# Optimization experiments

Hardware: AMD Instinct MI355X
Metric: run time of the kernel (lower is better)

## Reference

```python
import jax, jax.numpy as jnp
import numpy as np

INPUT_DIM = 128
OUTPUT_DIM = 128
FEATURE_DIM = 2 * OUTPUT_DIM            # 256
EDGE_DIM = 2 * FEATURE_DIM              # 512
H_DIM = INPUT_DIM + FEATURE_DIM + 2 * EDGE_DIM  # input + xp + (mean,max) pooled
N_INTT = 50000
N_MVTX = 50000
N_EDGES = 320000


def _linear_params(key, fan_in, fan_out):
    kw, kb = jax.random.split(key)
    lim = 1.0 / np.sqrt(fan_in)
    W = jax.random.uniform(kw, (fan_in, fan_out), jnp.float32, -lim, lim)
    b = jax.random.uniform(kb, (fan_out,), jnp.float32, -lim, lim)
    return W, b


def setup_inputs() -> dict:
    key = jax.random.key(0)
    ks = jax.random.split(key, 10)
    x_intt = jax.random.normal(ks[0], (N_INTT, INPUT_DIM), jnp.float32)
    x_mvtx = jax.random.normal(ks[1], (N_MVTX, INPUT_DIM), jnp.float32)
    start = jax.random.randint(ks[2], (N_EDGES,), 0, N_INTT)
    end = jax.random.randint(ks[3], (N_EDGES,), 0, N_MVTX)
    edge_index = jnp.stack([start, end], axis=0).astype(jnp.int64) if jax.config.jax_enable_x64 else jnp.stack([start, end], axis=0)
    W_in_intt, b_in_intt = _linear_params(ks[4], INPUT_DIM, FEATURE_DIM)
    W_in_mvtx, b_in_mvtx = _linear_params(ks[5], INPUT_DIM, FEATURE_DIM)
    W_score, b_score = _linear_params(ks[6], EDGE_DIM, 1)
    W_out_intt, b_out_intt = _linear_params(ks[7], H_DIM, OUTPUT_DIM)
    W_out_mvtx, b_out_mvtx = _linear_params(ks[8], H_DIM, OUTPUT_DIM)
    return {
        "x_intt": x_intt, "x_mvtx": x_mvtx, "edge_index": edge_index,
        "W_in_intt": W_in_intt, "b_in_intt": b_in_intt,
        "W_in_mvtx": W_in_mvtx, "b_in_mvtx": b_in_mvtx,
        "W_score": W_score, "b_score": b_score,
        "W_out_intt": W_out_intt, "b_out_intt": b_out_intt,
        "W_out_mvtx": W_out_mvtx, "b_out_mvtx": b_out_mvtx,
    }


def _scatter_mean(edges, idx, n):
    # torch_scatter.scatter_mean with out=zeros: sum / max(count, 1)
    s = jax.ops.segment_sum(edges, idx, num_segments=n)
    cnt = jax.ops.segment_sum(jnp.ones((edges.shape[0], 1), edges.dtype), idx, num_segments=n)
    return s / jnp.maximum(cnt, 1.0)


def _scatter_max(edges, idx, n):
    # torch_scatter.scatter_max with out=zeros: out participates in the max -> clamp at 0
    m = jax.ops.segment_max(edges, idx, num_segments=n)
    return jnp.maximum(m, 0.0)


def reference(x_intt, x_mvtx, edge_index,
              W_in_intt, b_in_intt, W_in_mvtx, b_in_mvtx,
              W_score, b_score, W_out_intt, b_out_intt,
              W_out_mvtx, b_out_mvtx):
    xp_intt = x_intt @ W_in_intt + b_in_intt          # [Ni, F]
    xp_mvtx = x_mvtx @ W_in_mvtx + b_in_mvtx          # [Nm, F]
    start, end = edge_index[0], edge_index[1]
    xp = jnp.concatenate([xp_intt[start], xp_mvtx[end]], axis=-1)  # [E, 2F]
    # aggregator_activation = 'potential': exp(-|x|)
    score = jnp.exp(-jnp.abs(xp @ W_score + b_score))  # [E, 1]
    edges = xp * score                                 # [E, 2F]

    mean_intt = _scatter_mean(edges, start, x_intt.shape[0])
    max_intt = _scatter_max(edges, start, x_intt.shape[0])
    mean_mvtx = _scatter_mean(edges, end, x_mvtx.shape[0])
    max_mvtx = _scatter_max(edges, end, x_mvtx.shape[0])

    H_intt = jnp.concatenate([x_intt, xp_intt, mean_intt, max_intt], axis=-1)
    H_mvtx = jnp.concatenate([x_mvtx, xp_mvtx, mean_mvtx, max_mvtx], axis=-1)
    h_intt = jax.nn.relu(H_intt @ W_out_intt + b_out_intt)
    h_mvtx = jax.nn.relu(H_mvtx @ W_out_mvtx + b_out_mvtx)
    return (h_intt, h_mvtx)
```

## Files before the change

### kernel.cpp

```cpp
#include <hip/hip_runtime.h>


typedef __attribute__((ext_vector_type(8))) short bf16x8;
typedef __attribute__((ext_vector_type(4))) float f32x4;

static __device__ __forceinline__ unsigned short f2bf(float f) {
  unsigned int u = __float_as_uint(f);
  u = (u + 0x7FFFu + ((u >> 16) & 1u)) >> 16;
  return (unsigned short)u;
}
static __device__ __forceinline__ float bf2f(unsigned short s) {
  return __uint_as_float(((unsigned int)s) << 16);
}

#define GLD16(gp, lp)                                                        \
  __builtin_amdgcn_global_load_lds(                                          \
      (const __attribute__((address_space(1))) void*)(gp),                   \
      (__attribute__((address_space(3))) void*)(lp), 16, 0, 0)

__global__ void k_prep_wt(const float* __restrict__ Wo,
                          unsigned short* __restrict__ Wt, int K, int Ncol) {
  int idx = blockIdx.x * blockDim.x + threadIdx.x;
  if (idx >= K * Ncol) return;
  int k = idx / Ncol, c = idx % Ncol;
  Wt[(size_t)c * K + k] = f2bf(Wo[idx]);
}

__global__ __launch_bounds__(256) void k_gemm_in(
    const float* __restrict__ x, const unsigned short* __restrict__ Wint,
    const float* __restrict__ bias, const float* __restrict__ Wsc,
    unsigned short* __restrict__ xp, float* __restrict__ a_out, int N) {
  __shared__ __align__(16) unsigned short Ab[64 * 16 * 8];
  __shared__ __align__(16) unsigned short Bb[256 * 16 * 8];
  const int tid = threadIdx.x;
  const int l = tid & 63;
  const int lr = l & 15, lg = l >> 4;
  const int w = tid >> 6, wr = w >> 1, wc = w & 1;
  const int r0 = blockIdx.x * 64;
  const int wbase = tid & 192;

#pragma unroll
  for (int i = 0; i < 16; ++i) {
    int g = i * 256 + tid;
    int row = g >> 4, c = g & 15;
    int sc = c ^ (row & 7);
    GLD16(Wint + (size_t)row * 128 + sc * 8,
          &Bb[(size_t)(i * 256 + wbase) * 8]);
  }
#pragma unroll
  for (int i = 0; i < 4; ++i) {
    int g = i * 256 + tid;
    int row = g >> 4, c = g & 15;
    int ar = min(r0 + row, N - 1);
    const float* src = x + (size_t)ar * 128 + c * 8;
    float4 u = *(const float4*)src;
    float4 v = *(const float4*)(src + 4);
    bf16x8 h;
    h[0] = (short)f2bf(u.x); h[1] = (short)f2bf(u.y);
    h[2] = (short)f2bf(u.z); h[3] = (short)f2bf(u.w);
    h[4] = (short)f2bf(v.x); h[5] = (short)f2bf(v.y);
    h[6] = (short)f2bf(v.z); h[7] = (short)f2bf(v.w);
    *(bf16x8*)&Ab[(size_t)(row * 16 + (c ^ (row & 7))) * 8] = h;
  }
  __syncthreads();

  f32x4 acc[2][8];
#pragma unroll
  for (int m = 0; m < 2; ++m)
#pragma unroll
    for (int t = 0; t < 8; ++t) {
      f32x4 z = {0.f, 0.f, 0.f, 0.f};
      acc[m][t] = z;
    }
#pragma unroll
  for (int kk = 0; kk < 4; ++kk) {
    int chq = kk * 4 + lg;
    bf16x8 a[2], bt[8];
#pragma unroll
    for (int m = 0; m < 2; ++m) {
      int row = wr * 32 + m * 16 + lr;
      a[m] = *(const bf16x8*)&Ab[(row * 16 + (chq ^ (row & 7))) * 8];
    }
#pragma unroll
    for (int t = 0; t < 8; ++t) {
      int row = wc * 128 + t * 16 + lr;
      bt[t] = *(const bf16x8*)&Bb[(row * 16 + (chq ^ (row & 7))) * 8];
    }
#pragma unroll
    for (int m = 0; m < 2; ++m)
#pragma unroll
      for (int t = 0; t < 8; ++t)
        acc[m][t] = __builtin_amdgcn_mfma_f32_16x16x32_bf16(
            a[m], bt[t], acc[m][t], 0, 0, 0);
  }

  float wscv[8], bb[8];
#pragma unroll
  for (int t = 0; t < 8; ++t) {
    int c = wc * 128 + t * 16 + lr;
    wscv[t] = Wsc[c];
    bb[t] = bias[c];
  }
#pragma unroll
  for (int m = 0; m < 2; ++m) {
    int rb = r0 + wr * 32 + m * 16 + lg * 4;
    float p0 = 0.f, p1 = 0.f, p2 = 0.f, p3 = 0.f;
#pragma unroll
    for (int t = 0; t < 8; ++t) {
      int c = wc * 128 + t * 16 + lr;
      float v0 = acc[m][t][0] + bb[t];
      float v1 = acc[m][t][1] + bb[t];
      float v2 = acc[m][t][2] + bb[t];
      float v3 = acc[m][t][3] + bb[t];
      if (rb + 0 < N) xp[(size_t)(rb + 0) * 256 + c] = f2bf(v0);
      if (rb + 1 < N) xp[(size_t)(rb + 1) * 256 + c] = f2bf(v1);
      if (rb + 2 < N) xp[(size_t)(rb + 2) * 256 + c] = f2bf(v2);
      if (rb + 3 < N) xp[(size_t)(rb + 3) * 256 + c] = f2bf(v3);
      p0 = fmaf(v0, wscv[t], p0); p1 = fmaf(v1, wscv[t], p1);
      p2 = fmaf(v2, wscv[t], p2); p3 = fmaf(v3, wscv[t], p3);
    }
#pragma unroll
    for (int off = 1; off < 16; off <<= 1) {
      p0 += __shfl_xor(p0, off); p1 += __shfl_xor(p1, off);
      p2 += __shfl_xor(p2, off); p3 += __shfl_xor(p3, off);
    }
    if (lr == 0) {
      if (rb + 0 < N) atomicAdd(a_out + rb + 0, p0);
      if (rb + 1 < N) atomicAdd(a_out + rb + 1, p1);
      if (rb + 2 < N) atomicAdd(a_out + rb + 2, p2);
      if (rb + 3 < N) atomicAdd(a_out + rb + 3, p3);
    }
  }
}

__global__ void k_deg(const int* __restrict__ es, const int* __restrict__ ee,
                      int E, int* __restrict__ deg_i, int* __restrict__ deg_m) {
  int e = blockIdx.x * blockDim.x + threadIdx.x;
  if (e >= E) return;
  atomicAdd(deg_i + es[e], 1);
  atomicAdd(deg_m + ee[e], 1);
}

__global__ __launch_bounds__(256) void k_scan_blk(
    const int* __restrict__ deg, int* __restrict__ blksum, int n) {
  __shared__ int sm[256];
  int t = threadIdx.x;
  int i = blockIdx.x * 256 + t;
  sm[t] = (i < n) ? deg[i] : 0;
  __syncthreads();
#pragma unroll
  for (int off = 128; off; off >>= 1) {
    if (t < off) sm[t] += sm[t + off];
    __syncthreads();
  }
  if (t == 0) blksum[blockIdx.x] = sm[0];
}

__global__ __launch_bounds__(1024) void k_scan_top(
    const int* __restrict__ bs_i, int* __restrict__ bb_i, int nbi,
    const int* __restrict__ bs_m, int* __restrict__ bb_m, int nbm) {
  const int* bs = blockIdx.x ? bs_m : bs_i;
  int* bb = blockIdx.x ? bb_m : bb_i;
  int nb = blockIdx.x ? nbm : nbi;
  __shared__ int sm[1024];
  int t = threadIdx.x;
  int d = (t < nb) ? bs[t] : 0;
  sm[t] = d;
  __syncthreads();
  for (int off = 1; off < 1024; off <<= 1) {
    int v = (t >= off) ? sm[t - off] : 0;
    __syncthreads();
    sm[t] += v;
    __syncthreads();
  }
  if (t < nb) bb[t] = sm[t] - d;
}

__global__ __launch_bounds__(256) void k_scan_wr(
    const int* __restrict__ deg, const int* __restrict__ blkbase,
    int* __restrict__ rp, int* __restrict__ cur, int n, int E) {
  __shared__ int sm[256];
  int t = threadIdx.x;
  int i = blockIdx.x * 256 + t;
  int d = (i < n) ? deg[i] : 0;
  sm[t] = d;
  __syncthreads();
  for (int off = 1; off < 256; off <<= 1) {
    int v = (t >= off) ? sm[t - off] : 0;
    __syncthreads();
    sm[t] += v;
    __syncthreads();
  }
  if (i < n) {
    int v = blkbase[blockIdx.x] + sm[t] - d;
    rp[i] = v; cur[i] = v;
  }
  if (i == 0) rp[n] = E;
}

__global__ void k_fill(const int* __restrict__ es, const int* __restrict__ ee,
                       int E, const float* __restrict__ a_i,
                       const float* __restrict__ a_m,
                       const float* __restrict__ bsc,
                       int* __restrict__ cur_i, int* __restrict__ col_i,
                       float* __restrict__ sv_i,
                       int* __restrict__ cur_m, int* __restrict__ col_m,
                       float* __restrict__ sv_m) {
  int e = blockIdx.x * blockDim.x + threadIdx.x;
  if (e >= E) return;
  int s = es[e], m = ee[e];
  float sc = expf(-fabsf(a_i[s] + a_m[m] + bsc[0]));
  int pi = atomicAdd(cur_i + s, 1);
  col_i[pi] = m; sv_i[pi] = sc;
  int pm = atomicAdd(cur_m + m, 1);
  col_m[pm] = s; sv_m[pm] = sc;
}

__global__ __launch_bounds__(256) void k_agg(
    const unsigned short* __restrict__ xp_oth,
    const int* __restrict__ rowptr, const int* __restrict__ col,
    const float* __restrict__ sv, unsigned short* __restrict__ Hg,
    float4* __restrict__ scal, int base, int cnt) {
  int local = blockIdx.x * 4 + (threadIdx.x >> 6);
  if (local >= cnt) return;
  int node = base + local;
  int l = threadIdx.x & 63;

  float sum_s = 0.f, mx_s = -1e30f, mn_s = 1e30f;
  float sv0 = 0.f, sv1 = 0.f, sv2 = 0.f, sv3 = 0.f;
  float mv0 = -1e30f, mv1 = -1e30f, mv2 = -1e30f, mv3 = -1e30f;
  int jb = rowptr[node], je = rowptr[node + 1];
  int dg = je - jb;
  int j = jb;
  for (; j + 3 < je; j += 4) {
    int o0 = col[j], o1 = col[j + 1], o2 = col[j + 2], o3 = col[j + 3];
    float s0 = sv[j], s1 = sv[j + 1], s2 = sv[j + 2], s3 = sv[j + 3];
    ushort4 g0 = *(const ushort4*)(xp_oth + (size_t)o0 * 256 + 4 * l);
    ushort4 g1 = *(const ushort4*)(xp_oth + (size_t)o1 * 256 + 4 * l);
    ushort4 g2 = *(const ushort4*)(xp_oth + (size_t)o2 * 256 + 4 * l);
    ushort4 g3 = *(const ushort4*)(xp_oth + (size_t)o3 * 256 + 4 * l);
    float f0, f1, f2, f3;
    f0 = bf2f(g0.x); f1 = bf2f(g0.y); f2 = bf2f(g0.z); f3 = bf2f(g0.w);
    sv0 = fmaf(s0, f0, sv0); sv1 = fmaf(s0, f1, sv1);
    sv2 = fmaf(s0, f2, sv2); sv3 = fmaf(s0, f3, sv3);
    mv0 = fmaxf(mv0, s0 * f0); mv1 = fmaxf(mv1, s0 * f1);
    mv2 = fmaxf(mv2, s0 * f2); mv3 = fmaxf(mv3, s0 * f3);
    f0 = bf2f(g1.x); f1 = bf2f(g1.y); f2 = bf2f(g1.z); f3 = bf2f(g1.w);
    sv0 = fmaf(s1, f0, sv0); sv1 = fmaf(s1, f1, sv1);
    sv2 = fmaf(s1, f2, sv2); sv3 = fmaf(s1, f3, sv3);
    mv0 = fmaxf(mv0, s1 * f0); mv1 = fmaxf(mv1, s1 * f1);
    mv2 = fmaxf(mv2, s1 * f2); mv3 = fmaxf(mv3, s1 * f3);
    f0 = bf2f(g2.x); f1 = bf2f(g2.y); f2 = bf2f(g2.z); f3 = bf2f(g2.w);
    sv0 = fmaf(s2, f0, sv0); sv1 = fmaf(s2, f1, sv1);
    sv2 = fmaf(s2, f2, sv2); sv3 = fmaf(s2, f3, sv3);
    mv0 = fmaxf(mv0, s2 * f0); mv1 = fmaxf(mv1, s2 * f1);
    mv2 = fmaxf(mv2, s2 * f2); mv3 = fmaxf(mv3, s2 * f3);
    f0 = bf2f(g3.x); f1 = bf2f(g3.y); f2 = bf2f(g3.z); f3 = bf2f(g3.w);
    sv0 = fmaf(s3, f0, sv0); sv1 = fmaf(s3, f1, sv1);
    sv2 = fmaf(s3, f2, sv2); sv3 = fmaf(s3, f3, sv3);
    mv0 = fmaxf(mv0, s3 * f0); mv1 = fmaxf(mv1, s3 * f1);
    mv2 = fmaxf(mv2, s3 * f2); mv3 = fmaxf(mv3, s3 * f3);
    sum_s += (s0 + s1) + (s2 + s3);
    mx_s = fmaxf(mx_s, fmaxf(fmaxf(s0, s1), fmaxf(s2, s3)));
    mn_s = fminf(mn_s, fminf(fminf(s0, s1), fminf(s2, s3)));
  }
  for (; j < je; ++j) {
    int o0 = col[j];
    float s0 = sv[j];
    ushort4 g0 = *(const ushort4*)(xp_oth + (size_t)o0 * 256 + 4 * l);
    float f0 = bf2f(g0.x), f1 = bf2f(g0.y), f2 = bf2f(g0.z), f3 = bf2f(g0.w);
    sv0 = fmaf(s0, f0, sv0); sv1 = fmaf(s0, f1, sv1);
    sv2 = fmaf(s0, f2, sv2); sv3 = fmaf(s0, f3, sv3);
    mv0 = fmaxf(mv0, s0 * f0); mv1 = fmaxf(mv1, s0 * f1);
    mv2 = fmaxf(mv2, s0 * f2); mv3 = fmaxf(mv3, s0 * f3);
    sum_s += s0; mx_s = fmaxf(mx_s, s0); mn_s = fminf(mn_s, s0);
  }
  float inv = 1.f / (float)(dg > 0 ? dg : 1);
  unsigned short* Hr = Hg + (size_t)local * 512;
  *(ushort4*)(Hr + 4 * l) = make_ushort4(
      f2bf(sv0 * inv), f2bf(sv1 * inv), f2bf(sv2 * inv), f2bf(sv3 * inv));
  *(ushort4*)(Hr + 256 + 4 * l) = make_ushort4(
      f2bf(fmaxf(mv0, 0.f)), f2bf(fmaxf(mv1, 0.f)),
      f2bf(fmaxf(mv2, 0.f)), f2bf(fmaxf(mv3, 0.f)));
  if (l == 0)
    scal[local] = make_float4(sum_s * inv, dg > 0 ? mx_s : 0.f,
                              dg > 0 ? mn_s : 0.f, 0.f);
}

__global__ __launch_bounds__(512) void k_gemm_out(
    const float* __restrict__ x, const unsigned short* __restrict__ xp,
    const unsigned short* __restrict__ Hg, const float4* __restrict__ scal,
    const unsigned short* __restrict__ Wt, const float* __restrict__ bias,
    float* __restrict__ out, int Nloc, int own_first) {
  __shared__ unsigned short Ab[2][64 * 64];
  __shared__ unsigned short Bb[2][128 * 64];
  const int tid = threadIdx.x;
  const int l = tid & 63;
  const int lr = l & 15, lg = l >> 4;
  const int w = tid >> 6;
  const int wr = w >> 2, wc = w & 3;
  const int r0 = blockIdx.x * 64;
  const int wbase = tid & 448;

  const int arow = tid >> 3, ac = tid & 7;
  const int ar = min(r0 + arow, Nloc - 1);
  const int asc = ac ^ (arow & 7);
  unsigned short* adst_reg = &Ab[0][(size_t)(arow * 8 + asc) * 8];
  const size_t adst_off = (size_t)(arow * 8 + asc) * 8;
  float4 s4 = scal[ar];
  const float ss = s4.x, mxs = s4.y, mns = s4.z;

  f32x4 acc[2][2];
#pragma unroll
  for (int m = 0; m < 2; ++m)
#pragma unroll
    for (int t = 0; t < 2; ++t) {
      f32x4 z = {0.f, 0.f, 0.f, 0.f};
      acc[m][t] = z;
    }

  auto stage = [&](int b, int t) {
    if (t < 2) {
      const float* src = x + (size_t)ar * 128 + t * 64 + ac * 8;
      float4 u = *(const float4*)src;
      float4 v = *(const float4*)(src + 4);
      bf16x8 h;
      h[0] = (short)f2bf(u.x); h[1] = (short)f2bf(u.y);
      h[2] = (short)f2bf(u.z); h[3] = (short)f2bf(u.w);
      h[4] = (short)f2bf(v.x); h[5] = (short)f2bf(v.y);
      h[6] = (short)f2bf(v.z); h[7] = (short)f2bf(v.w);
      *(bf16x8*)&Ab[b][adst_off] = h;
    } else if (t < 6) {
      GLD16(xp + (size_t)ar * 256 + (t - 2) * 64 + asc * 8,
            &Ab[b][(size_t)wbase * 8]);
    } else {
      int phase = (t - 6) >> 2, sub = (t - 6) & 3;
      int is_own = own_first ? !(phase & 1) : (phase & 1);
      if (is_own) {
        bf16x8 v = *(const bf16x8*)(xp + (size_t)ar * 256 + sub * 64 + ac * 8);
        bf16x8 h;
        if (phase < 2) {
#pragma unroll
          for (int i = 0; i < 8; ++i)
            h[i] = (short)f2bf(bf2f((unsigned short)v[i]) * ss);
        } else {
#pragma unroll
          for (int i = 0; i < 8; ++i) {
            float f = bf2f((unsigned short)v[i]);
            h[i] = (short)f2bf(fmaxf(fmaxf(f * mxs, f * mns), 0.f));
          }
        }
        *(bf16x8*)&Ab[b][adst_off] = h;
      } else {
        int hoff = (phase >= 2 ? 256 : 0) + sub * 64;
        GLD16(Hg + (size_t)ar * 512 + hoff + asc * 8,
              &Ab[b][(size_t)wbase * 8]);
      }
    }
    int kb = t * 64;
#pragma unroll
    for (int i = 0; i < 2; ++i) {
      int g = i * 512 + tid;
      int row = g >> 3, c = g & 7;
      int sc = c ^ (row & 7);
      GLD16(Wt + (size_t)row * 1408 + kb + sc * 8,
            &Bb[b][(size_t)(i * 512 + wbase) * 8]);
    }
  };

  auto compute = [&](int b) {
#pragma unroll
    for (int kk = 0; kk < 2; ++kk) {
      int chq = kk * 4 + lg;
      bf16x8 a[2], bt[2];
#pragma unroll
      for (int m = 0; m < 2; ++m) {
        int row = wr * 32 + m * 16 + lr;
        a[m] = *(const bf16x8*)&Ab[b][(row * 8 + (chq ^ (row & 7))) * 8];
      }
#pragma unroll
      for (int t = 0; t < 2; ++t) {
        int row = wc * 32 + t * 16 + lr;
        bt[t] = *(const bf16x8*)&Bb[b][(row * 8 + (chq ^ (row & 7))) * 8];
      }
#pragma unroll
      for (int m = 0; m < 2; ++m)
#pragma unroll
        for (int t = 0; t < 2; ++t)
          acc[m][t] = __builtin_amdgcn_mfma_f32_16x16x32_bf16(
              a[m], bt[t], acc[m][t], 0, 0, 0);
    }
  };

  stage(0, 0);
  __syncthreads();
  int cur = 0;
  for (int t = 0; t < 22; ++t) {
    if (t < 21) stage(cur ^ 1, t + 1);
    compute(cur);
    __syncthreads();
    cur ^= 1;
  }

#pragma unroll
  for (int m = 0; m < 2; ++m) {
    int rb = r0 + wr * 32 + m * 16 + lg * 4;
#pragma unroll
    for (int t = 0; t < 2; ++t) {
      int c = wc * 32 + t * 16 + lr;
      float bbias = bias[c];
#pragma unroll
      for (int r = 0; r < 4; ++r) {
        int rr = rb + r;
        if (rr < Nloc) out[(size_t)rr * 128 + c] = fmaxf(acc[m][t][r] + bbias, 0.f);
      }
    }
  }
}

extern "C" void kernel_launch(void* const* d_in, const int* in_sizes, int n_in,
                              void* d_out, int out_size, void* d_ws,
                              size_t ws_size, hipStream_t stream) {
  const float* x_i  = (const float*)d_in[0];
  const float* x_m  = (const float*)d_in[1];
  const int*   ei   = (const int*)d_in[2];
  const float* Wi_i = (const float*)d_in[3];
  const float* bi_i = (const float*)d_in[4];
  const float* Wi_m = (const float*)d_in[5];
  const float* bi_m = (const float*)d_in[6];
  const float* Wsc  = (const float*)d_in[7];
  const float* bsc  = (const float*)d_in[8];
  const float* Wo_i = (const float*)d_in[9];
  const float* bo_i = (const float*)d_in[10];
  const float* Wo_m = (const float*)d_in[11];
  const float* bo_m = (const float*)d_in[12];
  float* out = (float*)d_out;

  int Ni = in_sizes[0] / 128, Nm = in_sizes[1] / 128, E = in_sizes[2] / 2;
  const int* es = ei;
  const int* ee = ei + E;
  int nbi = (Ni + 255) / 256, nbm = (Nm + 255) / 256;

  char* p = (char*)d_ws;
  auto alloc = [&](size_t bytes) {
    char* q = p;
    p += (bytes + 255) & ~(size_t)255;
    return q;
  };
  unsigned short* xp_i = (unsigned short*)alloc((size_t)Ni * 256 * 2);
  unsigned short* xp_m = (unsigned short*)alloc((size_t)Nm * 256 * 2);
  float* a_i   = (float*)alloc((size_t)Ni * 4);
  float* a_m   = (float*)alloc((size_t)Nm * 4);
  int* deg_i   = (int*)alloc((size_t)Ni * 4);
  int* deg_m   = (int*)alloc((size_t)Nm * 4);
  int* rp_i    = (int*)alloc((size_t)(Ni + 1) * 4);
  int* rp_m    = (int*)alloc((size_t)(Nm + 1) * 4);
  int* cur_i   = (int*)alloc((size_t)Ni * 4);
  int* cur_m   = (int*)alloc((size_t)Nm * 4);
  int* bs_i    = (int*)alloc((size_t)nbi * 4);
  int* bs_m    = (int*)alloc((size_t)nbm * 4);
  int* bb_i    = (int*)alloc((size_t)nbi * 4);
  int* bb_m    = (int*)alloc((size_t)nbm * 4);
  int* col_i   = (int*)alloc((size_t)E * 4);
  int* col_m   = (int*)alloc((size_t)E * 4);
  float* sv_i  = (float*)alloc((size_t)E * 4);
  float* sv_m  = (float*)alloc((size_t)E * 4);
  unsigned short* Wt_i = (unsigned short*)alloc((size_t)128 * 1408 * 2);
  unsigned short* Wt_m = (unsigned short*)alloc((size_t)128 * 1408 * 2);
  unsigned short* Wint_i = (unsigned short*)alloc((size_t)256 * 128 * 2);
  unsigned short* Wint_m = (unsigned short*)alloc((size_t)256 * 128 * 2);

  size_t used = (size_t)(p - (char*)d_ws);
  if (used + 256 > ws_size) return;
  size_t avail = ws_size - used - 256;
  long long srows_ll = (long long)(avail / 1040);
  int maxN = (Ni > Nm ? Ni : Nm);
  int maxPad = (maxN + 127) & ~127;
  int S = (int)(srows_ll > maxPad ? maxPad : srows_ll);
  S &= ~127;
  if (S < 128) return;
  unsigned short* Hg = (unsigned short*)alloc((size_t)S * 512 * 2);
  float4* scal = (float4*)alloc((size_t)S * 16);

  hipMemsetAsync(deg_i, 0, (size_t)Ni * 4, stream);
  hipMemsetAsync(deg_m, 0, (size_t)Nm * 4, stream);
  hipMemsetAsync(a_i, 0, (size_t)Ni * 4, stream);
  hipMemsetAsync(a_m, 0, (size_t)Nm * 4, stream);

  k_prep_wt<<<(1408 * 128 + 255) / 256, 256, 0, stream>>>(Wo_i, Wt_i, 1408, 128);
  k_prep_wt<<<(1408 * 128 + 255) / 256, 256, 0, stream>>>(Wo_m, Wt_m, 1408, 128);
  k_prep_wt<<<(128 * 256 + 255) / 256, 256, 0, stream>>>(Wi_i, Wint_i, 128, 256);
  k_prep_wt<<<(128 * 256 + 255) / 256, 256, 0, stream>>>(Wi_m, Wint_m, 128, 256);

  k_gemm_in<<<(Ni + 63) / 64, 256, 0, stream>>>(x_i, Wint_i, bi_i, Wsc, xp_i, a_i, Ni);
  k_gemm_in<<<(Nm + 63) / 64, 256, 0, stream>>>(x_m, Wint_m, bi_m, Wsc + 256, xp_m, a_m, Nm);

  k_deg<<<(E + 255) / 256, 256, 0, stream>>>(es, ee, E, deg_i, deg_m);
  k_scan_blk<<<nbi, 256, 0, stream>>>(deg_i, bs_i, Ni);
  k_scan_blk<<<nbm, 256, 0, stream>>>(deg_m, bs_m, Nm);
  k_scan_top<<<2, 1024, 0, stream>>>(bs_i, bb_i, nbi, bs_m, bb_m, nbm);
  k_scan_wr<<<nbi, 256, 0, stream>>>(deg_i, bb_i, rp_i, cur_i, Ni, E);
  k_scan_wr<<<nbm, 256, 0, stream>>>(deg_m, bb_m, rp_m, cur_m, Nm, E);
  k_fill<<<(E + 255) / 256, 256, 0, stream>>>(es, ee, E, a_i, a_m, bsc,
                                              cur_i, col_i, sv_i,
                                              cur_m, col_m, sv_m);

  for (int base = 0; base < Ni; base += S) {
    int cnt = Ni - base; if (cnt > S) cnt = S;
    k_agg<<<(cnt + 3) / 4, 256, 0, stream>>>(xp_m, rp_i, col_i, sv_i,
                                             Hg, scal, base, cnt);
    k_gemm_out<<<(cnt + 63) / 64, 512, 0, stream>>>(
        x_i + (size_t)base * 128, xp_i + (size_t)base * 256, Hg, scal,
        Wt_i, bo_i, out + (size_t)base * 128, cnt, 1);
  }
  float* out_m = out + (size_t)Ni * 128;
  for (int base = 0; base < Nm; base += S) {
    int cnt = Nm - base; if (cnt > S) cnt = S;
    k_agg<<<(cnt + 3) / 4, 256, 0, stream>>>(xp_i, rp_m, col_m, sv_m,
                                             Hg, scal, base, cnt);
    k_gemm_out<<<(cnt + 63) / 64, 512, 0, stream>>>(
        x_m + (size_t)base * 128, xp_m + (size_t)base * 256, Hg, scal,
        Wt_m, bo_m, out_m + (size_t)base * 128, cnt, 0);
  }
}
```

Baseline: 292.1 us.

## Fuse GEMM of current slice with aggregation of next slice in one launch

New measurement: 288.6 us. About the same (-1.2%).

```diff
diff --git a/kernel.cpp b/kernel.cpp
--- a/kernel.cpp
+++ b/kernel.cpp
@@ -216,12 +216,12 @@
   col_m[pm] = s; sv_m[pm] = sc;
 }
 
-__global__ __launch_bounds__(256) void k_agg(
-    const unsigned short* __restrict__ xp_oth,
+static __device__ __forceinline__ void dev_agg(
+    int bid, const unsigned short* __restrict__ xp_oth,
     const int* __restrict__ rowptr, const int* __restrict__ col,
     const float* __restrict__ sv, unsigned short* __restrict__ Hg,
     float4* __restrict__ scal, int base, int cnt) {
-  int local = blockIdx.x * 4 + (threadIdx.x >> 6);
+  int local = bid * 8 + ((int)threadIdx.x >> 6);
   if (local >= cnt) return;
   int node = base + local;
   int l = threadIdx.x & 63;
@@ -287,8 +287,8 @@
                               dg > 0 ? mn_s : 0.f, 0.f);
 }
 
-__global__ __launch_bounds__(512) void k_gemm_out(
-    const float* __restrict__ x, const unsigned short* __restrict__ xp,
+static __device__ __forceinline__ void dev_gemm(
+    int bid, const float* __restrict__ x, const unsigned short* __restrict__ xp,
     const unsigned short* __restrict__ Hg, const float4* __restrict__ scal,
     const unsigned short* __restrict__ Wt, const float* __restrict__ bias,
     float* __restrict__ out, int Nloc, int own_first) {
@@ -299,13 +299,12 @@
   const int lr = l & 15, lg = l >> 4;
   const int w = tid >> 6;
   const int wr = w >> 2, wc = w & 3;
-  const int r0 = blockIdx.x * 64;
+  const int r0 = bid * 64;
   const int wbase = tid & 448;
 
   const int arow = tid >> 3, ac = tid & 7;
   const int ar = min(r0 + arow, Nloc - 1);
   const int asc = ac ^ (arow & 7);
-  unsigned short* adst_reg = &Ab[0][(size_t)(arow * 8 + asc) * 8];
   const size_t adst_off = (size_t)(arow * 8 + asc) * 8;
   float4 s4 = scal[ar];
   const float ss = s4.x, mxs = s4.y, mns = s4.z;
@@ -416,6 +415,29 @@
       }
     }
   }
+}
+
+__global__ __launch_bounds__(512) void k_agg8(
+    const unsigned short* __restrict__ xp_oth,
+    const int* __restrict__ rowptr, const int* __restrict__ col,
+    const float* __restrict__ sv, unsigned short* __restrict__ Hg,
+    float4* __restrict__ scal, int base, int cnt) {
+  dev_agg(blockIdx.x, xp_oth, rowptr, col, sv, Hg, scal, base, cnt);
+}
+
+__global__ __launch_bounds__(512) void k_fused(
+    const float* __restrict__ gx, const unsigned short* __restrict__ gxp,
+    const unsigned short* __restrict__ gHg, const float4* __restrict__ gscal,
+    const unsigned short* __restrict__ gWt, const float* __restrict__ gbias,
+    float* __restrict__ gout, int gN, int gown_first, int ngemm,
+    const unsigned short* __restrict__ axp, const int* __restrict__ arp,
+    const int* __restrict__ acol, const float* __restrict__ asv,
+    unsigned short* __restrict__ aHg, float4* __restrict__ ascal,
+    int abase, int acnt) {
+  if ((int)blockIdx.x < ngemm)
+    dev_gemm(blockIdx.x, gx, gxp, gHg, gscal, gWt, gbias, gout, gN, gown_first);
+  else
+    dev_agg(blockIdx.x - ngemm, axp, arp, acol, asv, aHg, ascal, abase, acnt);
 }
 
 extern "C" void kernel_launch(void* const* d_in, const int* in_sizes, int n_in,
@@ -473,14 +495,18 @@
   size_t used = (size_t)(p - (char*)d_ws);
   if (used + 256 > ws_size) return;
   size_t avail = ws_size - used - 256;
-  long long srows_ll = (long long)(avail / 1040);
+  long long srows_ll = (long long)(avail / 2080);
   int maxN = (Ni > Nm ? Ni : Nm);
   int maxPad = (maxN + 127) & ~127;
   int S = (int)(srows_ll > maxPad ? maxPad : srows_ll);
   S &= ~127;
   if (S < 128) return;
-  unsigned short* Hg = (unsigned short*)alloc((size_t)S * 512 * 2);
-  float4* scal = (float4*)alloc((size_t)S * 16);
+  unsigned short* HgB[2];
+  float4* scB[2];
+  HgB[0] = (unsigned short*)alloc((size_t)S * 512 * 2);
+  HgB[1] = (unsigned short*)alloc((size_t)S * 512 * 2);
+  scB[0] = (float4*)alloc((size_t)S * 16);
+  scB[1] = (float4*)alloc((size_t)S * 16);
 
   hipMemsetAsync(deg_i, 0, (size_t)Ni * 4, stream);
   hipMemsetAsync(deg_m, 0, (size_t)Nm * 4, stream);
@@ -505,21 +531,47 @@
                                               cur_i, col_i, sv_i,
                                               cur_m, col_m, sv_m);
 
-  for (int base = 0; base < Ni; base += S) {
-    int cnt = Ni - base; if (cnt > S) cnt = S;
-    k_agg<<<(cnt + 3) / 4, 256, 0, stream>>>(xp_m, rp_i, col_i, sv_i,
-                                             Hg, scal, base, cnt);
-    k_gemm_out<<<(cnt + 63) / 64, 512, 0, stream>>>(
-        x_i + (size_t)base * 128, xp_i + (size_t)base * 256, Hg, scal,
-        Wt_i, bo_i, out + (size_t)base * 128, cnt, 1);
-  }
-  float* out_m = out + (size_t)Ni * 128;
-  for (int base = 0; base < Nm; base += S) {
-    int cnt = Nm - base; if (cnt > S) cnt = S;
-    k_agg<<<(cnt + 3) / 4, 256, 0, stream>>>(xp_i, rp_m, col_m, sv_m,
-                                             Hg, scal, base, cnt);
-    k_gemm_out<<<(cnt + 63) / 64, 512, 0, stream>>>(
-        x_m + (size_t)base * 128, xp_m + (size_t)base * 256, Hg, scal,
-        Wt_m, bo_m, out_m + (size_t)base * 128, cnt, 0);
-  }
-}
+  int nsl = 0;
+  int sside[64], sbase[64], scnt[64];
+  for (int b = 0; b < Ni && nsl < 64; b += S) {
+    sside[nsl] = 0; sbase[nsl] = b;
+    scnt[nsl] = (Ni - b < S) ? Ni - b : S; ++nsl;
+  }
+  for (int b = 0; b < Nm && nsl < 64; b += S) {
+    sside[nsl] = 1; sbase[nsl] = b;
+    scnt[nsl] = (Nm - b < S) ? Nm - b : S; ++nsl;
+  }
+  const unsigned short* aggxp[2] = {xp_m, xp_i};
+  const int* rpT[2] = {rp_i, rp_m};
+  const int* colT[2] = {col_i, col_m};
+  const float* svT[2] = {sv_i, sv_m};
+  const float* xT[2] = {x_i, x_m};
+  const unsigned short* xpT[2] = {xp_i, xp_m};
+  const unsigned short* WtT[2] = {Wt_i, Wt_m};
+  const float* boT[2] = {bo_i, bo_m};
+  float* outT[2] = {out, out + (size_t)Ni * 128};
+  int ofT[2] = {1, 0};
+
+  {
+    int sd = sside[0];
+    k_agg8<<<(scnt[0] + 7) / 8, 512, 0, stream>>>(
+        aggxp[sd], rpT[sd], colT[sd], svT[sd], HgB[0], scB[0],
+        sbase[0], scnt[0]);
+  }
+  for (int k = 0; k < nsl; ++k) {
+    int sd = sside[k], bse = sbase[k], cnt = scnt[k];
+    int ngemm = (cnt + 63) / 64;
+    int nagg = 0;
+    int k1 = k + 1;
+    int sd1 = (k1 < nsl) ? sside[k1] : sd;
+    int b1 = (k1 < nsl) ? sbase[k1] : 0;
+    int c1 = (k1 < nsl) ? scnt[k1] : 0;
+    if (k1 < nsl) nagg = (c1 + 7) / 8;
+    k_fused<<<ngemm + nagg, 512, 0, stream>>>(
+        xT[sd] + (size_t)bse * 128, xpT[sd] + (size_t)bse * 256,
+        HgB[k & 1], scB[k & 1], WtT[sd], boT[sd],
+        outT[sd] + (size_t)bse * 128, cnt, ofT[sd], ngemm,
+        aggxp[sd1], rpT[sd1], colT[sd1], svT[sd1],
+        HgB[k1 & 1], scB[k1 & 1], b1, c1);
+  }
+}
```
